# Performance work log

Hardware: AMD Instinct MI355X
Metric: run time of the kernel (lower is better)

## Reference

```python
import jax, jax.numpy as jnp
import numpy as np

N = 50000      # query points
M = 50000      # support points
KNN = 32       # neighbors per query
K = 15         # kernel points
C_IN = 64
C_OUT = 128
RADIUS = 2.5
KP_EXTENT = 1.2


def setup_inputs() -> dict:
    key = jax.random.key(0)
    ks = jax.random.split(key, 6)
    q_pts = jax.random.uniform(ks[0], (N, 3), dtype=jnp.float32)
    s_pts = jax.random.uniform(ks[1], (M, 3), dtype=jnp.float32)
    s_feats = jax.random.normal(ks[2], (M, C_IN), dtype=jnp.float32)
    # index M refers to the appended shadow point/feature row
    neigh_inds = jax.random.randint(ks[3], (N, KNN), 0, M + 1, dtype=jnp.int32)
    weights = jax.random.normal(ks[4], (K, C_IN, C_OUT), dtype=jnp.float32) * 0.05
    kernel_points = (jax.random.uniform(ks[5], (K, 3), dtype=jnp.float32) * 2.0 - 1.0) * RADIUS
    return {"q_pts": q_pts, "s_pts": s_pts, "s_feats": s_feats,
            "neigh_inds": neigh_inds, "weights": weights,
            "kernel_points": kernel_points}


def reference(q_pts, s_pts, s_feats, neigh_inds, weights, kernel_points):
    # append shadow point far away and zero shadow feature row
    s_pts_pad = jnp.concatenate([s_pts, jnp.full((1, 3), 1e6, s_pts.dtype)], axis=0)
    s_feats_pad = jnp.concatenate(
        [s_feats, jnp.zeros((1, s_feats.shape[1]), s_feats.dtype)], axis=0)

    neigh_pts = s_pts_pad[neigh_inds] - q_pts[:, None, :]       # (n, k, 3)
    neigh_feats = s_feats_pad[neigh_inds]                        # (n, k, c_in)

    diff = neigh_pts[:, :, None, :] - kernel_points[None, None]  # (n, k, K, 3)
    sq_dist = jnp.sum(diff * diff, axis=-1) + 1e-8               # (n, k, K)

    # linear kernel-point influence
    h = jnp.clip(1.0 - jnp.sqrt(sq_dist) / KP_EXTENT, 0.0)       # (n, k, K)

    # aggregate neighbor feats per kernel point, then apply per-kernel weights
    kernel_feats = jnp.einsum('nke,nkc->nec', h, neigh_feats)    # (n, K, c_in)
    q_feats = jnp.einsum('nec,eco->no', kernel_feats, weights)   # (n, c_out)

    # normalize by number of valid (non-shadow, sum>0) neighbors
    neighbor_num = jnp.sum(jnp.sum(neigh_feats, axis=-1) > 0, axis=-1)
    neighbor_num = jnp.maximum(neighbor_num, 1).astype(q_feats.dtype)[:, None]
    return q_feats / neighbor_num
```

## Files before the change

kernel.cpp:

```cpp
#include <hip/hip_runtime.h>


namespace {
constexpr int NQ   = 50000;
constexpr int MS   = 50000;
constexpr int KNN  = 32;
constexpr int KP   = 15;
constexpr int CIN  = 64;
constexpr int COUT = 128;
constexpr int QB   = 32;
constexpr int ROWS = KP * CIN;
constexpr int RND  = 3;
constexpr int RE   = 5;
constexpr int KBR  = (RE * CIN) / 32;
constexpr int KBT  = ROWS / 32;
constexpr int ASTR = RE * CIN + 4;
constexpr float KP_EXT_INV = 1.0f / 1.2f;
constexpr int OF_CPK = 0;
constexpr int OF_KP  = 256;
constexpr size_t WSB_HI  = 200704;
constexpr size_t WSB_LO  = 446464;
constexpr size_t WSB_END = 692224;
}

typedef __attribute__((ext_vector_type(8))) short short8;
typedef __attribute__((ext_vector_type(4))) float f32x4;
typedef __attribute__((ext_vector_type(4))) unsigned int u32x4;

__device__ __forceinline__ short f32_bf16(float x) {
    unsigned u = __builtin_bit_cast(unsigned, x);
    u = u + 0x7fffu + ((u >> 16) & 1u);
    return (short)(u >> 16);
}
__device__ __forceinline__ float bf16_f32(short h) {
    unsigned u = ((unsigned)(unsigned short)h) << 16;
    return __builtin_bit_cast(float, u);
}
__device__ __forceinline__ unsigned pack_hilo(float x) {
    unsigned xu = __builtin_bit_cast(unsigned, x);
    unsigned r  = xu + 0x7fffu + ((xu >> 16) & 1u);
    unsigned hi = r & 0xffff0000u;
    float lof = x - __builtin_bit_cast(float, hi);
    unsigned lu = __builtin_bit_cast(unsigned, lof);
    unsigned r2 = lu + 0x7fffu + ((lu >> 16) & 1u);
    return hi | (r2 >> 16);
}
__device__ __forceinline__ unsigned permb(unsigned a, unsigned b, unsigned sel) {
#if __has_builtin(__builtin_amdgcn_perm)
    return __builtin_amdgcn_perm(a, b, sel);
#else
    if (sel == 0x07060302u) return (a & 0xffff0000u) | (b >> 16);
    return (a << 16) | (b & 0xffffu);
#endif
}
__device__ __forceinline__ void unpack8(uint4 a, uint4 b, short8& hi, short8& lo) {
    u32x4 h, l;
    h[0] = permb(a.y, a.x, 0x07060302u); l[0] = permb(a.y, a.x, 0x05040100u);
    h[1] = permb(a.w, a.z, 0x07060302u); l[1] = permb(a.w, a.z, 0x05040100u);
    h[2] = permb(b.y, b.x, 0x07060302u); l[2] = permb(b.y, b.x, 0x05040100u);
    h[3] = permb(b.w, b.z, 0x07060302u); l[3] = permb(b.w, b.z, 0x05040100u);
    hi = __builtin_bit_cast(short8, h);
    lo = __builtin_bit_cast(short8, l);
}
__device__ __forceinline__ float readlane_f(float v, int l) {
    return __builtin_bit_cast(float,
        __builtin_amdgcn_readlane(__builtin_bit_cast(int, v), l));
}

__global__ __launch_bounds__(256)
void prep_basic(const float* __restrict__ s_feats, const float* __restrict__ W,
                float* __restrict__ rs, short* __restrict__ whi, short* __restrict__ wlo)
{
    int b = blockIdx.x;
    if (b < 60) {
        int wv = threadIdx.x >> 6, lane = threadIdx.x & 63;
        int id = b * 4 + wv;
        int t = id / KBT, kb = id % KBT;
        short8 hi8, lo8;
        #pragma unroll
        for (int j = 0; j < 8; ++j) {
            int row = kb * 32 + ((lane >> 4) & 3) * 8 + j;
            int col = t * 16 + (lane & 15);
            float x = W[(size_t)row * COUT + col];
            short h = f32_bf16(x);
            hi8[j] = h;
            lo8[j] = f32_bf16(x - bf16_f32(h));
        }
        ((short8*)whi)[id * 64 + lane] = hi8;
        ((short8*)wlo)[id * 64 + lane] = lo8;
    } else {
        int tdx = (b - 60) * 256 + threadIdx.x;
        int row = tdx >> 3, l8 = tdx & 7;
        if (row < MS) {
            const float4* p = (const float4*)(s_feats + (size_t)row * CIN + l8 * 8);
            float4 a = p[0], c = p[1];
            float s = ((a.x + a.y) + (a.z + a.w)) + ((c.x + c.y) + (c.z + c.w));
            s += __shfl_xor(s, 1);
            s += __shfl_xor(s, 2);
            s += __shfl_xor(s, 4);
            if (l8 == 0) rs[row] = s;
        }
    }
}

__global__ __launch_bounds__(512, 4)
void kpconv_mfma(const float* __restrict__ q_pts,
                 const float* __restrict__ s_pts,
                 const float* __restrict__ s_feats,
                 const int*   __restrict__ neigh,
                 const float* __restrict__ kpts,
                 const float* __restrict__ rowsum,
                 const short* __restrict__ whi,
                 const short* __restrict__ wlo,
                 float*       __restrict__ out)
{
    __shared__ __align__(16) unsigned int smem[QB * ASTR];
    __shared__ float norm_s[QB];

    float* smf = (float*)smem;
    const int tid  = threadIdx.x;
    const int lane = tid & 63;
    const int wv   = tid >> 6;
    const int blk  = blockIdx.x;
    const int k32  = lane & 31;
    const int half = lane >> 5;
    const int quad = lane >> 4;
    const int c15  = lane & 15;

    int*   cpk  = (int*)(smf + OF_CPK) + wv * 32;
    float* kp_s = smf + OF_KP;

    if (tid < KP * 3) kp_s[tid] = kpts[tid];
    __syncthreads();

    float kfv[4][KP];

    #pragma unroll
    for (int j = 0; j < 4; ++j) {
        const int q  = wv * 4 + j;
        const int n  = blk * QB + q;
        const int nc = n < NQ ? n : NQ - 1;
        const float qx = q_pts[nc * 3 + 0];
        const float qy = q_pts[nc * 3 + 1];
        const float qz = q_pts[nc * 3 + 2];

        int  idxv  = neigh[nc * KNN + k32];
        bool valid = idxv < MS;
        int  icv   = valid ? idxv : MS - 1;
        float px = s_pts[icv * 3 + 0];
        float py = s_pts[icv * 3 + 1];
        float pz = s_pts[icv * 3 + 2];
        float dx = valid ? px - qx : 1e6f;
        float dy = valid ? py - qy : 1e6f;
        float dz = valid ? pz - qz : 1e6f;
        bool flag = valid && (rowsum[icv] > 0.0f);
        {
            unsigned long long b = __ballot(flag);
            int cnt = (int)(__popcll(b) >> 1);
            if (lane == 0) norm_s[q] = 1.0f / (float)(cnt > 1 ? cnt : 1);
        }

        float hreg[8];
        float om = 0.0f;
        #pragma unroll
        for (int p = 0; p < 8; ++p) {
            const int e = (p << 1) + half;
            float hh = 0.0f;
            if (e < KP) {
                float ax = dx - kp_s[e * 3 + 0];
                float ay = dy - kp_s[e * 3 + 1];
                float az = dz - kp_s[e * 3 + 2];
                float d2 = ax * ax + ay * ay + az * az + 1e-8f;
                hh = 1.0f - sqrtf(d2) * KP_EXT_INV;
                hh = hh > 0.0f ? hh : 0.0f;
            }
            hreg[p] = hh;
            om = fmaxf(om, hh);
        }
        om = fmaxf(om, __shfl_xor(om, 32));
        unsigned int kmask = (unsigned int)__ballot(om > 0.0f);
        const int nv = __popc(kmask);

        if (lane < KNN) {
            bool bit = (kmask >> k32) & 1u;
            unsigned lm = (1u << k32) - 1u;
            int pos = bit ? __popc(kmask & lm) : nv + __popc((~kmask) & lm);
            cpk[pos] = bit ? ((idxv << 6) | k32) : 0;
        }
        __builtin_amdgcn_wave_barrier();

        #pragma unroll
        for (int e = 0; e < KP; ++e) kfv[j][e] = 0.0f;

        const int nvr = (nv + 3) & ~3;
        for (int base = 0; base < nvr; base += 4) {
            int pk[4];
            float nf[4];
            #pragma unroll
            for (int u = 0; u < 4; ++u) pk[u] = __builtin_amdgcn_readfirstlane(cpk[base + u]);
            #pragma unroll
            for (int u = 0; u < 4; ++u) nf[u] = s_feats[(size_t)(pk[u] >> 6) * CIN + lane];
            #pragma unroll
            for (int u = 0; u < 4; ++u) {
                nf[u] = (base + u < nv) ? nf[u] : 0.0f;
                const int kk = pk[u] & 63;
                float f = nf[u];
                #pragma unroll
                for (int e = 0; e < KP; ++e) {
                    float he = readlane_f(hreg[e >> 1], kk | ((e & 1) << 5));
                    kfv[j][e] += he * f;
                }
            }
        }
    }

    const short8* wh = (const short8*)whi;
    const short8* wl = (const short8*)wlo;
    f32x4 acc0 = {0.f, 0.f, 0.f, 0.f};
    f32x4 acc1 = {0.f, 0.f, 0.f, 0.f};
    const int qA = c15;

    #pragma unroll
    for (int r = 0; r < RND; ++r) {
        __syncthreads();
        #pragma unroll
        for (int j = 0; j < 4; ++j) {
            const int qrow = (4 * wv + j) * ASTR;
            #pragma unroll
            for (int e5 = 0; e5 < RE; ++e5) {
                smem[qrow + e5 * CIN + lane] = pack_hilo(kfv[j][r * RE + e5]);
            }
        }
        __syncthreads();

        #pragma unroll 2
        for (int kb = 0; kb < KBR; ++kb) {
            const uint4* a0p = (const uint4*)(smem + qA * ASTR + kb * 32 + quad * 8);
            uint4 a0 = a0p[0], a0b = a0p[1];
            const uint4* a1p = (const uint4*)(smem + (16 + qA) * ASTR + kb * 32 + quad * 8);
            uint4 a1 = a1p[0], a1b = a1p[1];
            short8 ah0, al0, ah1, al1;
            unpack8(a0, a0b, ah0, al0);
            unpack8(a1, a1b, ah1, al1);

            const int kbg = r * KBR + kb;
            short8 bh = wh[(wv * KBT + kbg) * 64 + lane];
            short8 bl = wl[(wv * KBT + kbg) * 64 + lane];

            acc0 = __builtin_amdgcn_mfma_f32_16x16x32_bf16(ah0, bh, acc0, 0, 0, 0);
            acc1 = __builtin_amdgcn_mfma_f32_16x16x32_bf16(ah1, bh, acc1, 0, 0, 0);
            acc0 = __builtin_amdgcn_mfma_f32_16x16x32_bf16(ah0, bl, acc0, 0, 0, 0);
            acc1 = __builtin_amdgcn_mfma_f32_16x16x32_bf16(ah1, bl, acc1, 0, 0, 0);
            acc0 = __builtin_amdgcn_mfma_f32_16x16x32_bf16(al0, bh, acc0, 0, 0, 0);
            acc1 = __builtin_amdgcn_mfma_f32_16x16x32_bf16(al1, bh, acc1, 0, 0, 0);
        }
    }

    const int oc = c15;
    #pragma unroll
    for (int rr = 0; rr < 4; ++rr) {
        int qm0 = quad * 4 + rr;
        int qm1 = 16 + qm0;
        int n0 = blk * QB + qm0;
        int n1 = blk * QB + qm1;
        if (n0 < NQ) out[(size_t)n0 * COUT + wv * 16 + oc] = acc0[rr] * norm_s[qm0];
        if (n1 < NQ) out[(size_t)n1 * COUT + wv * 16 + oc] = acc1[rr] * norm_s[qm1];
    }
}

__global__ __launch_bounds__(256, 6)
void kpconv_fallback(const float* __restrict__ q_pts,
                     const float* __restrict__ s_pts,
                     const float* __restrict__ s_feats,
                     const int*   __restrict__ neigh,
                     const float* __restrict__ W,
                     const float* __restrict__ kpts,
                     float*       __restrict__ out)
{
    constexpr int QBF = 16, CHUNK_I = 320, NPAIR = 160;
    __shared__ __align__(16) float smem[NPAIR * 32];
    __shared__ float norm_s[QBF];
    float (*h_lds)[KNN][20] = (float (*)[KNN][20])smem;
    float (*dxyz)[KNN][3]   = (float (*)[KNN][3])(smem + 2560);
    int*   idxl             = (int*)(smem + 2944);
    float* kp_s             = smem + 3072;

    const int tid = threadIdx.x, lane = tid & 63, wv = tid >> 6, blk = blockIdx.x;
    const int k32 = lane & 31, half = lane >> 5;
    if (tid < KP * 3) kp_s[tid] = kpts[tid];
    __syncthreads();
    float kfv[4][KP];

    #pragma unroll
    for (int j = 0; j < 4; ++j) {
        const int q = wv * 4 + j, n = blk * QBF + q;
        const float qx = q_pts[n*3], qy = q_pts[n*3+1], qz = q_pts[n*3+2];
        if (lane < KNN) {
            int idx = neigh[n * KNN + k32];
            idxl[wv * KNN + k32] = idx;
            bool valid = idx < MS;
            int ic = valid ? idx : MS - 1;
            dxyz[wv][k32][0] = valid ? s_pts[ic*3]   - qx : 1e6f;
            dxyz[wv][k32][1] = valid ? s_pts[ic*3+1] - qy : 1e6f;
            dxyz[wv][k32][2] = valid ? s_pts[ic*3+2] - qz : 1e6f;
        }
        __builtin_amdgcn_wave_barrier();
        const float dx = dxyz[wv][k32][0], dy = dxyz[wv][k32][1], dz = dxyz[wv][k32][2];
        float om = 0.0f;
        #pragma unroll
        for (int p = 0; p < 8; ++p) {
            const int e = (p << 1) + half;
            if (e < KP) {
                float ax = dx - kp_s[e*3], ay = dy - kp_s[e*3+1], az = dz - kp_s[e*3+2];
                float hh = 1.0f - sqrtf(ax*ax + ay*ay + az*az + 1e-8f) * KP_EXT_INV;
                hh = hh > 0.0f ? hh : 0.0f;
                h_lds[wv][k32][e] = hh;
                om = fmaxf(om, hh);
            }
        }
        om = fmaxf(om, __shfl_xor(om, 32));
        unsigned int kmask = (unsigned int)__ballot(om > 0.0f);
        __builtin_amdgcn_wave_barrier();
        {
            int idx = idxl[wv * KNN + k32];
            bool valid = idx < MS;
            int ic = valid ? idx : MS - 1;
            const float4* rp = (const float4*)(s_feats + (size_t)ic * CIN + half * 32);
            float4 s4 = rp[0];
            #pragma unroll
            for (int t = 1; t < 8; ++t) { float4 a = rp[t]; s4.x+=a.x; s4.y+=a.y; s4.z+=a.z; s4.w+=a.w; }
            float s = (s4.x + s4.y) + (s4.z + s4.w);
            s += __shfl_xor(s, 32);
            unsigned long long b = __ballot(valid && (s > 0.0f));
            int cnt = (int)(__popcll(b) >> 1);
            if (lane == 0) norm_s[q] = 1.0f / (float)(cnt > 1 ? cnt : 1);
        }
        #pragma unroll
        for (int e = 0; e < KP; ++e) kfv[j][e] = 0.0f;
        unsigned int mk = kmask;
        while (mk) {
            int k = __builtin_ctz(mk); mk &= mk - 1;
            int idx2 = idxl[wv * KNN + k];
            int ic2 = idx2 < MS ? idx2 : MS - 1;
            float nf = s_feats[(size_t)ic2 * CIN + lane];
            const float4* hr = (const float4*)(&h_lds[wv][k][0]);
            float4 h0 = hr[0], h1 = hr[1], h2 = hr[2], h3 = hr[3];
            kfv[j][0]+=h0.x*nf; kfv[j][1]+=h0.y*nf; kfv[j][2]+=h0.z*nf; kfv[j][3]+=h0.w*nf;
            kfv[j][4]+=h1.x*nf; kfv[j][5]+=h1.y*nf; kfv[j][6]+=h1.z*nf; kfv[j][7]+=h1.w*nf;
            kfv[j][8]+=h2.x*nf; kfv[j][9]+=h2.y*nf; kfv[j][10]+=h2.z*nf; kfv[j][11]+=h2.w*nf;
            kfv[j][12]+=h3.x*nf; kfv[j][13]+=h3.y*nf; kfv[j][14]+=h3.z*nf;
        }
    }

    const int o4 = tid & 31, qi = tid >> 5, q0 = qi * 2, q1 = q0 + 1;
    float4 tot0 = make_float4(0,0,0,0), tot1 = make_float4(0,0,0,0);
    #pragma unroll
    for (int r = 0; r < 3; ++r) {
        __syncthreads();
        #pragma unroll
        for (int j = 0; j < 4; ++j) {
            const int q = wv * 4 + j;
            #pragma unroll
            for (int e5 = 0; e5 < 5; ++e5) {
                int i = e5 * CIN + lane, pr = i >> 1, m = pr & 14;
                smem[pr * 32 + ((q ^ m) << 1) + (i & 1)] = kfv[j][r * 5 + e5];
            }
        }
        __syncthreads();
        const float* wb = W + (size_t)(r * CHUNK_I) * COUT + (o4 << 2);
        float4 acc0 = make_float4(0,0,0,0), acc1 = make_float4(0,0,0,0);
        #pragma unroll 4
        for (int p = 0; p < NPAIR; ++p) {
            float4 kk = *(const float4*)(smem + p * 32 + ((q0 ^ (p & 14)) << 1));
            float4 w0 = *(const float4*)(wb + (size_t)(2*p) * COUT);
            float4 w1 = *(const float4*)(wb + (size_t)(2*p+1) * COUT);
            acc0.x+=w0.x*kk.x; acc0.y+=w0.y*kk.x; acc0.z+=w0.z*kk.x; acc0.w+=w0.w*kk.x;
            acc1.x+=w0.x*kk.z; acc1.y+=w0.y*kk.z; acc1.z+=w0.z*kk.z; acc1.w+=w0.w*kk.z;
            acc0.x+=w1.x*kk.y; acc0.y+=w1.y*kk.y; acc0.z+=w1.z*kk.y; acc0.w+=w1.w*kk.y;
            acc1.x+=w1.x*kk.w; acc1.y+=w1.y*kk.w; acc1.z+=w1.z*kk.w; acc1.w+=w1.w*kk.w;
        }
        tot0.x+=acc0.x; tot0.y+=acc0.y; tot0.z+=acc0.z; tot0.w+=acc0.w;
        tot1.x+=acc1.x; tot1.y+=acc1.y; tot1.z+=acc1.z; tot1.w+=acc1.w;
    }
    const float nm0 = norm_s[q0], nm1 = norm_s[q1];
    const size_t base = (size_t)(blk * QBF) * COUT + (o4 << 2);
    *(float4*)(out + base + (size_t)q0 * COUT) =
        make_float4(tot0.x*nm0, tot0.y*nm0, tot0.z*nm0, tot0.w*nm0);
    *(float4*)(out + base + (size_t)q1 * COUT) =
        make_float4(tot1.x*nm1, tot1.y*nm1, tot1.z*nm1, tot1.w*nm1);
}

extern "C" void kernel_launch(void* const* d_in, const int* in_sizes, int n_in,
                              void* d_out, int out_size, void* d_ws, size_t ws_size,
                              hipStream_t stream) {
    const float* q_pts   = (const float*)d_in[0];
    const float* s_pts   = (const float*)d_in[1];
    const float* s_feats = (const float*)d_in[2];
    const int*   neigh   = (const int*)d_in[3];
    const float* W       = (const float*)d_in[4];
    const float* kpts    = (const float*)d_in[5];
    float* outp = (float*)d_out;

    dim3 mgrid((NQ + QB - 1) / QB);
    dim3 mblock(512);

    if (ws_size >= WSB_END) {
        float* rs  = (float*)d_ws;
        short* whi = (short*)((char*)d_ws + WSB_HI);
        short* wlo = (short*)((char*)d_ws + WSB_LO);
        int rs_blocks = (MS * 8 + 255) / 256;
        hipLaunchKernelGGL(prep_basic, dim3(60 + rs_blocks), dim3(256), 0, stream,
                           s_feats, W, rs, whi, wlo);
        hipLaunchKernelGGL(kpconv_mfma, mgrid, mblock, 0, stream,
                           q_pts, s_pts, s_feats, neigh, kpts, rs, whi, wlo, outp);
    } else {
        hipLaunchKernelGGL(kpconv_fallback, dim3(NQ / 16), dim3(256), 0, stream,
                           q_pts, s_pts, s_feats, neigh, W, kpts, outp);
    }
}
```

Before: 157.9 us.

## Split hi/lo bf16 planes in LDS, hoist point loads, prefetch neighbor features

```diff
diff --git a/kernel.cpp b/kernel.cpp
--- a/kernel.cpp
+++ b/kernel.cpp
@@ -14,7 +14,8 @@
 constexpr int RE   = 5;
 constexpr int KBR  = (RE * CIN) / 32;
 constexpr int KBT  = ROWS / 32;
-constexpr int ASTR = RE * CIN + 4;
+constexpr int SRH  = 328;
+constexpr int LO_OFF = QB * SRH;
 constexpr float KP_EXT_INV = 1.0f / 1.2f;
 constexpr int OF_CPK = 0;
 constexpr int OF_KP  = 256;
@@ -25,7 +26,6 @@
 
 typedef __attribute__((ext_vector_type(8))) short short8;
 typedef __attribute__((ext_vector_type(4))) float f32x4;
-typedef __attribute__((ext_vector_type(4))) unsigned int u32x4;
 
 __device__ __forceinline__ short f32_bf16(float x) {
     unsigned u = __builtin_bit_cast(unsigned, x);
@@ -35,32 +35,6 @@
 __device__ __forceinline__ float bf16_f32(short h) {
     unsigned u = ((unsigned)(unsigned short)h) << 16;
     return __builtin_bit_cast(float, u);
-}
-__device__ __forceinline__ unsigned pack_hilo(float x) {
-    unsigned xu = __builtin_bit_cast(unsigned, x);
-    unsigned r  = xu + 0x7fffu + ((xu >> 16) & 1u);
-    unsigned hi = r & 0xffff0000u;
-    float lof = x - __builtin_bit_cast(float, hi);
-    unsigned lu = __builtin_bit_cast(unsigned, lof);
-    unsigned r2 = lu + 0x7fffu + ((lu >> 16) & 1u);
-    return hi | (r2 >> 16);
-}
-__device__ __forceinline__ unsigned permb(unsigned a, unsigned b, unsigned sel) {
-#if __has_builtin(__builtin_amdgcn_perm)
-    return __builtin_amdgcn_perm(a, b, sel);
-#else
-    if (sel == 0x07060302u) return (a & 0xffff0000u) | (b >> 16);
-    return (a << 16) | (b & 0xffffu);
-#endif
-}
-__device__ __forceinline__ void unpack8(uint4 a, uint4 b, short8& hi, short8& lo) {
-    u32x4 h, l;
-    h[0] = permb(a.y, a.x, 0x07060302u); l[0] = permb(a.y, a.x, 0x05040100u);
-    h[1] = permb(a.w, a.z, 0x07060302u); l[1] = permb(a.w, a.z, 0x05040100u);
-    h[2] = permb(b.y, b.x, 0x07060302u); l[2] = permb(b.y, b.x, 0x05040100u);
-    h[3] = permb(b.w, b.z, 0x07060302u); l[3] = permb(b.w, b.z, 0x05040100u);
-    hi = __builtin_bit_cast(short8, h);
-    lo = __builtin_bit_cast(short8, l);
 }
 __device__ __forceinline__ float readlane_f(float v, int l) {
     return __builtin_bit_cast(float,
@@ -114,17 +88,17 @@
                  const short* __restrict__ wlo,
                  float*       __restrict__ out)
 {
-    __shared__ __align__(16) unsigned int smem[QB * ASTR];
+    __shared__ __align__(16) short smem_s[2 * QB * SRH];
     __shared__ float norm_s[QB];
 
-    float* smf = (float*)smem;
+    float* smf = (float*)smem_s;
     const int tid  = threadIdx.x;
     const int lane = tid & 63;
     const int wv   = tid >> 6;
     const int blk  = blockIdx.x;
     const int k32  = lane & 31;
+    const int quad = lane >> 4;
     const int half = lane >> 5;
-    const int quad = lane >> 4;
     const int c15  = lane & 15;
 
     int*   cpk  = (int*)(smf + OF_CPK) + wv * 32;
@@ -135,30 +109,42 @@
 
     float kfv[4][KP];
 
+    float dxa[4], dya[4], dza[4];
+    int   idxa[4];
+    {
+        int nca[4];
+        #pragma unroll
+        for (int j = 0; j < 4; ++j) {
+            const int n = blk * QB + wv * 4 + j;
+            nca[j] = n < NQ ? n : NQ - 1;
+        }
+        #pragma unroll
+        for (int j = 0; j < 4; ++j) idxa[j] = neigh[nca[j] * KNN + k32];
+        #pragma unroll
+        for (int j = 0; j < 4; ++j) {
+            const float qx = q_pts[nca[j] * 3 + 0];
+            const float qy = q_pts[nca[j] * 3 + 1];
+            const float qz = q_pts[nca[j] * 3 + 2];
+            bool valid = idxa[j] < MS;
+            int  icv   = valid ? idxa[j] : MS - 1;
+            float px = s_pts[icv * 3 + 0];
+            float py = s_pts[icv * 3 + 1];
+            float pz = s_pts[icv * 3 + 2];
+            float rsv = rowsum[icv];
+            dxa[j] = valid ? px - qx : 1e6f;
+            dya[j] = valid ? py - qy : 1e6f;
+            dza[j] = valid ? pz - qz : 1e6f;
+            bool flag = valid && (rsv > 0.0f);
+            unsigned long long b = __ballot(flag);
+            int cnt = (int)(__popcll(b) >> 1);
+            if (lane == 0) norm_s[wv * 4 + j] = 1.0f / (float)(cnt > 1 ? cnt : 1);
+        }
+    }
+
     #pragma unroll
     for (int j = 0; j < 4; ++j) {
-        const int q  = wv * 4 + j;
-        const int n  = blk * QB + q;
-        const int nc = n < NQ ? n : NQ - 1;
-        const float qx = q_pts[nc * 3 + 0];
-        const float qy = q_pts[nc * 3 + 1];
-        const float qz = q_pts[nc * 3 + 2];
-
-        int  idxv  = neigh[nc * KNN + k32];
-        bool valid = idxv < MS;
-        int  icv   = valid ? idxv : MS - 1;
-        float px = s_pts[icv * 3 + 0];
-        float py = s_pts[icv * 3 + 1];
-        float pz = s_pts[icv * 3 + 2];
-        float dx = valid ? px - qx : 1e6f;
-        float dy = valid ? py - qy : 1e6f;
-        float dz = valid ? pz - qz : 1e6f;
-        bool flag = valid && (rowsum[icv] > 0.0f);
-        {
-            unsigned long long b = __ballot(flag);
-            int cnt = (int)(__popcll(b) >> 1);
-            if (lane == 0) norm_s[q] = 1.0f / (float)(cnt > 1 ? cnt : 1);
-        }
+        const float dx = dxa[j], dy = dya[j], dz = dza[j];
+        const int idxv = idxa[j];
 
         float hreg[8];
         float om = 0.0f;
@@ -193,24 +179,37 @@
         for (int e = 0; e < KP; ++e) kfv[j][e] = 0.0f;
 
         const int nvr = (nv + 3) & ~3;
+        int   pkc[4];
+        float nfc[4];
+        #pragma unroll
+        for (int u = 0; u < 4; ++u) pkc[u] = __builtin_amdgcn_readfirstlane(cpk[u]);
+        #pragma unroll
+        for (int u = 0; u < 4; ++u) nfc[u] = s_feats[(size_t)(pkc[u] >> 6) * CIN + lane];
+
         for (int base = 0; base < nvr; base += 4) {
-            int pk[4];
-            float nf[4];
-            #pragma unroll
-            for (int u = 0; u < 4; ++u) pk[u] = __builtin_amdgcn_readfirstlane(cpk[base + u]);
-            #pragma unroll
-            for (int u = 0; u < 4; ++u) nf[u] = s_feats[(size_t)(pk[u] >> 6) * CIN + lane];
+            int   pkn[4];
+            float nfn[4];
             #pragma unroll
             for (int u = 0; u < 4; ++u) {
-                nf[u] = (base + u < nv) ? nf[u] : 0.0f;
-                const int kk = pk[u] & 63;
-                float f = nf[u];
+                int ii = base + 4 + u;
+                ii = ii < 31 ? ii : 31;
+                pkn[u] = __builtin_amdgcn_readfirstlane(cpk[ii]);
+            }
+            #pragma unroll
+            for (int u = 0; u < 4; ++u) nfn[u] = s_feats[(size_t)(pkn[u] >> 6) * CIN + lane];
+
+            #pragma unroll
+            for (int u = 0; u < 4; ++u) {
+                const float f = (base + u < nv) ? nfc[u] : 0.0f;
+                const int   kk = pkc[u] & 63;
                 #pragma unroll
                 for (int e = 0; e < KP; ++e) {
                     float he = readlane_f(hreg[e >> 1], kk | ((e & 1) << 5));
                     kfv[j][e] += he * f;
                 }
             }
+            #pragma unroll
+            for (int u = 0; u < 4; ++u) { pkc[u] = pkn[u]; nfc[u] = nfn[u]; }
         }
     }
 
@@ -225,23 +224,25 @@
         __syncthreads();
         #pragma unroll
         for (int j = 0; j < 4; ++j) {
-            const int qrow = (4 * wv + j) * ASTR;
+            const int q = 4 * wv + j;
             #pragma unroll
             for (int e5 = 0; e5 < RE; ++e5) {
-                smem[qrow + e5 * CIN + lane] = pack_hilo(kfv[j][r * RE + e5]);
+                float v  = kfv[j][r * RE + e5];
+                short hi = f32_bf16(v);
+                short lo = f32_bf16(v - bf16_f32(hi));
+                smem_s[q * SRH + e5 * 64 + lane]          = hi;
+                smem_s[LO_OFF + q * SRH + e5 * 64 + lane] = lo;
             }
         }
         __syncthreads();
 
         #pragma unroll 2
         for (int kb = 0; kb < KBR; ++kb) {
-            const uint4* a0p = (const uint4*)(smem + qA * ASTR + kb * 32 + quad * 8);
-            uint4 a0 = a0p[0], a0b = a0p[1];
-            const uint4* a1p = (const uint4*)(smem + (16 + qA) * ASTR + kb * 32 + quad * 8);
-            uint4 a1 = a1p[0], a1b = a1p[1];
-            short8 ah0, al0, ah1, al1;
-            unpack8(a0, a0b, ah0, al0);
-            unpack8(a1, a1b, ah1, al1);
+            const int ai = kb * 32 + quad * 8;
+            short8 ah0 = *(const short8*)(smem_s + qA * SRH + ai);
+            short8 al0 = *(const short8*)(smem_s + LO_OFF + qA * SRH + ai);
+            short8 ah1 = *(const short8*)(smem_s + (16 + qA) * SRH + ai);
+            short8 al1 = *(const short8*)(smem_s + LO_OFF + (16 + qA) * SRH + ai);
 
             const int kbg = r * KBR + kb;
             short8 bh = wh[(wv * KBT + kbg) * 64 + lane];
```

Result: no change. 156.0 us (-1.2%).
